# Kernel optimization log

Measured on AMD Instinct MI355X. Metric: run time of the kernel, lower is better.

## Reference

```python
import jax, jax.numpy as jnp
import numpy as np

# MiniCPM3 MLA attention dims
HIDDEN = 2560
N_HEADS = 40
Q_LORA = 768
KV_LORA = 256
ROPE_D = 32
NOPE_D = 64
V_D = HIDDEN // N_HEADS          # 64
Q_HEAD_D = NOPE_D + ROPE_D       # 96
ROPE_BASE = 10000.0
EPS = 1e-6


def setup_inputs() -> dict:
    key = jax.random.key(0)
    ks = jax.random.split(key, 8)
    B, S = 1, 2048
    sc = lambda fan_in: 1.0 / np.sqrt(fan_in)
    return {
        "hidden_states": jax.random.normal(ks[0], (B, S, HIDDEN), jnp.float32),
        "position_ids": jnp.arange(B * S, dtype=jnp.int64).reshape(B, S) % S,
        "w_qa": jax.random.normal(ks[1], (HIDDEN, Q_LORA), jnp.float32) * sc(HIDDEN),
        "q_a_ln_w": jnp.ones((Q_LORA,), jnp.float32),
        "w_qb": jax.random.normal(ks[2], (Q_LORA, N_HEADS * Q_HEAD_D), jnp.float32) * sc(Q_LORA),
        "w_kva": jax.random.normal(ks[3], (HIDDEN, KV_LORA + ROPE_D), jnp.float32) * sc(HIDDEN),
        "kv_a_ln_w": jnp.ones((KV_LORA,), jnp.float32),
        "w_kvb": jax.random.normal(ks[4], (KV_LORA, N_HEADS * (NOPE_D + V_D)), jnp.float32) * sc(KV_LORA),
        "w_o": jax.random.normal(ks[5], (N_HEADS * V_D, HIDDEN), jnp.float32) * sc(N_HEADS * V_D),
    }


def _rmsnorm(x, w, eps=EPS):
    var = jnp.mean(x * x, axis=-1, keepdims=True)
    return x * jax.lax.rsqrt(var + eps) * w


def _rotate_half(x):
    h = x.shape[-1] // 2
    return jnp.concatenate([-x[..., h:], x[..., :h]], axis=-1)


def _rope_cache(seq_len, dim, base, dtype=jnp.float32):
    inv_freq = 1.0 / (base ** (jnp.arange(0, dim, 2, dtype=jnp.float32) / dim))
    t = jnp.arange(seq_len, dtype=jnp.float32)
    freqs = jnp.outer(t, inv_freq)                      # [S, dim/2]
    emb = jnp.concatenate([freqs, freqs], axis=-1)      # [S, dim]
    return jnp.cos(emb).astype(dtype), jnp.sin(emb).astype(dtype)


def reference(hidden_states, position_ids, w_qa, q_a_ln_w, w_qb, w_kva, kv_a_ln_w, w_kvb, w_o):
    B, S, _ = hidden_states.shape
    # --- low-rank Q projection: a -> RMSNorm -> b ---
    q = _rmsnorm(hidden_states @ w_qa, q_a_ln_w) @ w_qb          # [B,S,H*96]
    q = q.reshape(B, S, N_HEADS, Q_HEAD_D).transpose(0, 2, 1, 3)  # [B,H,S,96]
    q_nope, q_pe = q[..., :NOPE_D], q[..., NOPE_D:]
    # --- compressed KV + shared rope key ---
    ckv = hidden_states @ w_kva                                   # [B,S,256+32]
    compressed_kv, k_pe = ckv[..., :KV_LORA], ckv[..., KV_LORA:]
    k_pe = k_pe[:, None, :, :]                                    # [B,1,S,32]
    kv = _rmsnorm(compressed_kv, kv_a_ln_w) @ w_kvb               # [B,S,H*(64+64)]
    kv = kv.reshape(B, S, N_HEADS, NOPE_D + V_D).transpose(0, 2, 1, 3)
    k_nope, v = kv[..., :NOPE_D], kv[..., NOPE_D:]                # [B,H,S,64] each
    # --- RoPE on the 32-dim rope sub-dimension (fp32, as original) ---
    cos, sin = _rope_cache(S, ROPE_D, ROPE_BASE)
    cos = cos[position_ids][:, None, :, :]                        # [B,1,S,32]
    sin = sin[position_ids][:, None, :, :]
    q_pe = q_pe * cos + _rotate_half(q_pe) * sin
    k_pe = k_pe * cos + _rotate_half(k_pe) * sin
    # --- concat nope/rope parts ---
    q_full = jnp.concatenate([q_nope, q_pe], axis=-1)             # [B,H,S,96]
    k_full = jnp.concatenate([k_nope, jnp.broadcast_to(k_pe, (B, N_HEADS, S, ROPE_D))], axis=-1)
    # --- causal SDPA with scale q_head_dim**-0.5 ---
    scale = Q_HEAD_D ** -0.5
    scores = jnp.einsum("bhqd,bhkd->bhqk", q_full, k_full) * scale
    causal = jnp.tril(jnp.ones((S, S), bool))
    scores = jnp.where(causal, scores, jnp.finfo(scores.dtype).min)
    probs = jax.nn.softmax(scores, axis=-1)
    attn = jnp.einsum("bhqk,bhkd->bhqd", probs, v)                # [B,H,S,64]
    attn = attn.transpose(0, 2, 1, 3).reshape(B, S, N_HEADS * V_D)
    return attn @ w_o
```

## Files before the change

kernel.cpp:

```cpp
#include <hip/hip_runtime.h>
#include <hip/hip_bf16.h>

typedef __hip_bfloat16 bf16;
typedef __attribute__((ext_vector_type(8))) __bf16 bf16x8;
typedef __attribute__((ext_vector_type(4))) __bf16 bf16x4;
typedef __attribute__((ext_vector_type(4))) float f32x4;

constexpr int S_LEN = 2048;
constexpr int HID   = 2560;
constexpr int NH    = 40;
constexpr int QL    = 768;
constexpr int KVL   = 256;
constexpr int RD    = 32;
constexpr int ND    = 64;
constexpr int VD    = 64;
constexpr int QHD   = 96;
constexpr int QB_N  = NH * QHD;
constexpr int KVB_N = NH * (ND + VD);
constexpr int CKV_N = KVL + RD;
constexpr int AB_N  = QL + CKV_N;

#define MFMA16(a, b, c) __builtin_amdgcn_mfma_f32_16x16x32_bf16((a), (b), (c), 0, 0, 0)

__device__ __forceinline__ int get_pos(const int* pos, int s) {
  bool is64 = (pos[1] == 0 && pos[2] == 1);
  return is64 ? pos[2 * s] : pos[s];
}


__global__ void cast_f32_bf16(const float* __restrict__ src, bf16* __restrict__ dst, int n4) {
  int i = blockIdx.x * blockDim.x + threadIdx.x;
  if (i >= n4) return;
  float4 v = reinterpret_cast<const float4*>(src)[i];
  struct { bf16 a, b, c, d; } pk;
  pk.a = __float2bfloat16(v.x); pk.b = __float2bfloat16(v.y);
  pk.c = __float2bfloat16(v.z); pk.d = __float2bfloat16(v.w);
  reinterpret_cast<uint2*>(dst)[i] = *reinterpret_cast<uint2*>(&pk);
}

__global__ void transpose_cast(const float* __restrict__ src, bf16* __restrict__ dst, int K, int N) {
  __shared__ float tile[32][33];
  int nb = blockIdx.x * 32, kb = blockIdx.y * 32;
  int x = threadIdx.x, y = threadIdx.y;
#pragma unroll
  for (int j = 0; j < 4; ++j) {
    int k = kb + y + j * 8, n = nb + x;
    tile[y + j * 8][x] = (k < K && n < N) ? src[(size_t)k * N + n] : 0.f;
  }
  __syncthreads();
#pragma unroll
  for (int j = 0; j < 4; ++j) {
    int n = nb + y + j * 8, k = kb + x;
    if (n < N && k < K) dst[(size_t)n * K + k] = __float2bfloat16(tile[x][y + j * 8]);
  }
}


template<bool OBF16, bool NEDGE>
__global__ __launch_bounds__(256) void gemm_bt(const bf16* __restrict__ A,
                                               const bf16* __restrict__ B,
                                               void* __restrict__ Cv,
                                               int M, int N, int K) {
  constexpr int BM = 128, BN = 128, BK = 64;
  __shared__ __bf16 ldsA[BM * BK];
  __shared__ __bf16 ldsB[BN * BK];
  const int t = threadIdx.x;
  const int l = t & 63, w = t >> 6;
  const int lr = l & 15, lk = l >> 4;
  const int wr = w >> 1, wc = w & 1;
  const int rowbase = blockIdx.y * BM;
  const int colbase = blockIdx.x * BN;

  f32x4 acc[4][4];
#pragma unroll
  for (int m = 0; m < 4; ++m)
#pragma unroll
    for (int n = 0; n < 4; ++n) acc[m][n] = f32x4{0.f, 0.f, 0.f, 0.f};

  const int kiters = K / BK;
  for (int kt = 0; kt < kiters; ++kt) {
    const int kb = kt * BK;
#pragma unroll
    for (int it = 0; it < 4; ++it) {
      const int r  = it * 32 + w * 8 + (l >> 3);
      const int c8 = ((l & 7) * 8) ^ ((r & 7) << 3);
      const bf16* ga = A + (size_t)(rowbase + r) * K + kb + c8;
      __builtin_amdgcn_global_load_lds((const __attribute__((address_space(1))) void*)ga,
          (__attribute__((address_space(3))) void*)(ldsA + it * 2048 + w * 512), 16, 0, 0);
      int nrow = colbase + r;
      if (NEDGE) nrow = (nrow < N) ? nrow : (N - 1);
      const bf16* gb = B + (size_t)nrow * K + kb + c8;
      __builtin_amdgcn_global_load_lds((const __attribute__((address_space(1))) void*)gb,
          (__attribute__((address_space(3))) void*)(ldsB + it * 2048 + w * 512), 16, 0, 0);
    }
    __syncthreads();
#pragma unroll
    for (int kk = 0; kk < 2; ++kk) {
      bf16x8 af[4], bfr[4];
#pragma unroll
      for (int m = 0; m < 4; ++m) {
        const int row = wr * 64 + m * 16 + lr;
        const int ce  = (kk * 32 + lk * 8) ^ ((row & 7) << 3);
        af[m] = *(const bf16x8*)(ldsA + row * BK + ce);
      }
#pragma unroll
      for (int n = 0; n < 4; ++n) {
        const int row = wc * 64 + n * 16 + lr;
        const int ce  = (kk * 32 + lk * 8) ^ ((row & 7) << 3);
        bfr[n] = *(const bf16x8*)(ldsB + row * BK + ce);
      }
#pragma unroll
      for (int m = 0; m < 4; ++m)
#pragma unroll
        for (int n = 0; n < 4; ++n)
          acc[m][n] = MFMA16(af[m], bfr[n], acc[m][n]);
    }
    __syncthreads();
  }

#pragma unroll
  for (int m = 0; m < 4; ++m)
#pragma unroll
    for (int n = 0; n < 4; ++n) {
      const int col = colbase + wc * 64 + n * 16 + lr;
      if (NEDGE && col >= N) continue;
#pragma unroll
      for (int i = 0; i < 4; ++i) {
        const int row = rowbase + wr * 64 + m * 16 + lk * 4 + i;
        if (OBF16) ((bf16*)Cv)[(size_t)row * N + col] = __float2bfloat16(acc[m][n][i]);
        else       ((float*)Cv)[(size_t)row * N + col] = acc[m][n][i];
      }
    }
}

__global__ __launch_bounds__(256) void gemm_qakva(const bf16* __restrict__ A,
                                                  const bf16* __restrict__ B,
                                                  float* __restrict__ q_out,
                                                  float* __restrict__ ckv_out) {
  constexpr int BM = 128, BK = 64, K = HID, N = AB_N;
  __shared__ __bf16 ldsA[BM * BK];
  __shared__ __bf16 ldsB[64 * BK];
  const int t = threadIdx.x;
  const int l = t & 63, w = t >> 6;
  const int lr = l & 15, lk = l >> 4;
  const int rowbase = blockIdx.y * BM;
  const int colbase = blockIdx.x * 64;

  f32x4 acc[2][4];
#pragma unroll
  for (int m = 0; m < 2; ++m)
#pragma unroll
    for (int n = 0; n < 4; ++n) acc[m][n] = f32x4{0.f, 0.f, 0.f, 0.f};

  for (int kt = 0; kt < K / BK; ++kt) {
    const int kb = kt * BK;
#pragma unroll
    for (int it = 0; it < 4; ++it) {
      const int r  = it * 32 + w * 8 + (l >> 3);
      const int c8 = ((l & 7) * 8) ^ ((r & 7) << 3);
      const bf16* ga = A + (size_t)(rowbase + r) * K + kb + c8;
      __builtin_amdgcn_global_load_lds((const __attribute__((address_space(1))) void*)ga,
          (__attribute__((address_space(3))) void*)(ldsA + it * 2048 + w * 512), 16, 0, 0);
      if (it < 2) {
        int nrow = colbase + r;
        nrow = (nrow < N) ? nrow : (N - 1);
        const bf16* gb = B + (size_t)nrow * K + kb + c8;
        __builtin_amdgcn_global_load_lds((const __attribute__((address_space(1))) void*)gb,
            (__attribute__((address_space(3))) void*)(ldsB + it * 2048 + w * 512), 16, 0, 0);
      }
    }
    __syncthreads();
#pragma unroll
    for (int kk = 0; kk < 2; ++kk) {
      bf16x8 af[2], bfr[4];
#pragma unroll
      for (int m = 0; m < 2; ++m) {
        const int row = w * 32 + m * 16 + lr;
        const int ce  = (kk * 32 + lk * 8) ^ ((row & 7) << 3);
        af[m] = *(const bf16x8*)(ldsA + row * BK + ce);
      }
#pragma unroll
      for (int n = 0; n < 4; ++n) {
        const int row = n * 16 + lr;
        const int ce  = (kk * 32 + lk * 8) ^ ((row & 7) << 3);
        bfr[n] = *(const bf16x8*)(ldsB + row * BK + ce);
      }
#pragma unroll
      for (int m = 0; m < 2; ++m)
#pragma unroll
        for (int n = 0; n < 4; ++n)
          acc[m][n] = MFMA16(af[m], bfr[n], acc[m][n]);
    }
    __syncthreads();
  }

#pragma unroll
  for (int m = 0; m < 2; ++m)
#pragma unroll
    for (int n = 0; n < 4; ++n) {
      const int col = colbase + n * 16 + lr;
#pragma unroll
      for (int i = 0; i < 4; ++i) {
        const int row = rowbase + w * 32 + m * 16 + lk * 4 + i;
        if (col < QL)       q_out[(size_t)row * QL + col] = acc[m][n][i];
        else if (col < N)   ckv_out[(size_t)row * CKV_N + (col - QL)] = acc[m][n][i];
      }
    }
}

__global__ __launch_bounds__(256) void gemm_qb_rope(const bf16* __restrict__ A,
                                                    const bf16* __restrict__ B,
                                                    const float* __restrict__ ropc,
                                                    const float* __restrict__ rops,
                                                    bf16* __restrict__ qfull) {
  constexpr int BM = 128, BN = 128, BK = 64, K = QL, N = QB_N;
  __shared__ __bf16 ldsA[BM * BK];
  __shared__ __bf16 ldsB[BN * BK];
  const int t = threadIdx.x;
  const int l = t & 63, w = t >> 6;
  const int lr = l & 15, lk = l >> 4;
  const int wr = w >> 1, wc = w & 1;
  const int rowbase = blockIdx.y * BM;
  const int colbase = blockIdx.x * BN;
  const float scale = 0.14724444f;

  f32x4 acc[4][4];
#pragma unroll
  for (int m = 0; m < 4; ++m)
#pragma unroll
    for (int n = 0; n < 4; ++n) acc[m][n] = f32x4{0.f, 0.f, 0.f, 0.f};

  for (int kt = 0; kt < K / BK; ++kt) {
    const int kb = kt * BK;
#pragma unroll
    for (int it = 0; it < 4; ++it) {
      const int r  = it * 32 + w * 8 + (l >> 3);
      const int c8 = ((l & 7) * 8) ^ ((r & 7) << 3);
      const bf16* ga = A + (size_t)(rowbase + r) * K + kb + c8;
      __builtin_amdgcn_global_load_lds((const __attribute__((address_space(1))) void*)ga,
          (__attribute__((address_space(3))) void*)(ldsA + it * 2048 + w * 512), 16, 0, 0);
      const bf16* gb = B + (size_t)(colbase + r) * K + kb + c8;
      __builtin_amdgcn_global_load_lds((const __attribute__((address_space(1))) void*)gb,
          (__attribute__((address_space(3))) void*)(ldsB + it * 2048 + w * 512), 16, 0, 0);
    }
    __syncthreads();
#pragma unroll
    for (int kk = 0; kk < 2; ++kk) {
      bf16x8 af[4], bfr[4];
#pragma unroll
      for (int m = 0; m < 4; ++m) {
        const int row = wr * 64 + m * 16 + lr;
        const int ce  = (kk * 32 + lk * 8) ^ ((row & 7) << 3);
        af[m] = *(const bf16x8*)(ldsA + row * BK + ce);
      }
#pragma unroll
      for (int n = 0; n < 4; ++n) {
        const int row = wc * 64 + n * 16 + lr;
        const int ce  = (kk * 32 + lk * 8) ^ ((row & 7) << 3);
        bfr[n] = *(const bf16x8*)(ldsB + row * BK + ce);
      }
#pragma unroll
      for (int m = 0; m < 4; ++m)
#pragma unroll
        for (int n = 0; n < 4; ++n)
          acc[m][n] = MFMA16(af[m], bfr[n], acc[m][n]);
    }
    __syncthreads();
  }

#pragma unroll
  for (int m = 0; m < 4; ++m) {
    const int rowtop = rowbase + wr * 64 + m * 16 + lk * 4;
#pragma unroll
    for (int n = 0; n < 4; ++n) {
      const int c0 = colbase + wc * 64 + n * 16;
      const int h  = c0 / 96;
      const int d0 = c0 - h * 96;
      const size_t qb_ = ((size_t)h * S_LEN + rowtop) * QHD + d0 + lr;
      if (d0 < ND) {
#pragma unroll
        for (int i = 0; i < 4; ++i)
          qfull[qb_ + (size_t)i * QHD] = __float2bfloat16(acc[m][n][i] * scale);
      } else if (d0 == ND) {
#pragma unroll
        for (int i = 0; i < 4; ++i) {
          const float c = ropc[(rowtop + i) * 16 + lr];
          const float s = rops[(rowtop + i) * 16 + lr];
          const float x0 = acc[m][n][i], x1 = acc[m][n + 1][i];
          qfull[qb_ + (size_t)i * QHD] = __float2bfloat16((x0 * c - x1 * s) * scale);
        }
      } else {
#pragma unroll
        for (int i = 0; i < 4; ++i) {
          const float c = ropc[(rowtop + i) * 16 + lr];
          const float s = rops[(rowtop + i) * 16 + lr];
          const float x1 = acc[m][n][i], x0 = acc[m][n - 1][i];
          qfull[qb_ + (size_t)i * QHD] = __float2bfloat16((x1 * c + x0 * s) * scale);
        }
      }
    }
  }
}

__global__ __launch_bounds__(256) void gemm_kvb_split(const bf16* __restrict__ A,
                                                      const bf16* __restrict__ B,
                                                      bf16* __restrict__ knope,
                                                      bf16* __restrict__ vt) {
  constexpr int BM = 128, BN = 128, BK = 64, K = KVL;
  __shared__ __bf16 ldsA[BM * BK];
  __shared__ __bf16 ldsB[BN * BK];
  const int t = threadIdx.x;
  const int l = t & 63, w = t >> 6;
  const int lr = l & 15, lk = l >> 4;
  const int wr = w >> 1, wc = w & 1;
  const int rowbase = blockIdx.y * BM;
  const int h = blockIdx.x;
  const int colbase = h * BN;

  f32x4 acc[4][4];
#pragma unroll
  for (int m = 0; m < 4; ++m)
#pragma unroll
    for (int n = 0; n < 4; ++n) acc[m][n] = f32x4{0.f, 0.f, 0.f, 0.f};

  for (int kt = 0; kt < K / BK; ++kt) {
    const int kb = kt * BK;
#pragma unroll
    for (int it = 0; it < 4; ++it) {
      const int r  = it * 32 + w * 8 + (l >> 3);
      const int c8 = ((l & 7) * 8) ^ ((r & 7) << 3);
      const bf16* ga = A + (size_t)(rowbase + r) * K + kb + c8;
      __builtin_amdgcn_global_load_lds((const __attribute__((address_space(1))) void*)ga,
          (__attribute__((address_space(3))) void*)(ldsA + it * 2048 + w * 512), 16, 0, 0);
      const bf16* gb = B + (size_t)(colbase + r) * K + kb + c8;
      __builtin_amdgcn_global_load_lds((const __attribute__((address_space(1))) void*)gb,
          (__attribute__((address_space(3))) void*)(ldsB + it * 2048 + w * 512), 16, 0, 0);
    }
    __syncthreads();
#pragma unroll
    for (int kk = 0; kk < 2; ++kk) {
      bf16x8 af[4], bfr[4];
#pragma unroll
      for (int m = 0; m < 4; ++m) {
        const int row = wr * 64 + m * 16 + lr;
        const int ce  = (kk * 32 + lk * 8) ^ ((row & 7) << 3);
        af[m] = *(const bf16x8*)(ldsA + row * BK + ce);
      }
#pragma unroll
      for (int n = 0; n < 4; ++n) {
        const int row = wc * 64 + n * 16 + lr;
        const int ce  = (kk * 32 + lk * 8) ^ ((row & 7) << 3);
        bfr[n] = *(const bf16x8*)(ldsB + row * BK + ce);
      }
#pragma unroll
      for (int m = 0; m < 4; ++m)
#pragma unroll
        for (int n = 0; n < 4; ++n)
          acc[m][n] = MFMA16(af[m], bfr[n], acc[m][n]);
    }
    __syncthreads();
  }

#pragma unroll
  for (int m = 0; m < 4; ++m) {
    const int rowtop = rowbase + wr * 64 + m * 16 + lk * 4;
    if (wc == 0) {
#pragma unroll
      for (int n = 0; n < 4; ++n) {
        const int d = n * 16 + lr;
#pragma unroll
        for (int i = 0; i < 4; ++i)
          knope[((size_t)h * S_LEN + rowtop + i) * ND + d] = __float2bfloat16(acc[m][n][i]);
      }
    } else {
#pragma unroll
      for (int n = 0; n < 4; ++n) {
        const int d = n * 16 + lr;
        bf16x4 pk;
#pragma unroll
        for (int i = 0; i < 4; ++i) pk[i] = (__bf16)acc[m][n][i];
        *(bf16x4*)(vt + ((size_t)h * VD + d) * S_LEN + rowtop) = pk;
      }
    }
  }
}


__global__ void rmsnorm_rows(const float* __restrict__ in, const float* __restrict__ w,
                             bf16* __restrict__ out, int C) {
  const int r = blockIdx.x;
  const float* row = in + (size_t)r * C;
  float ss = 0.f;
  for (int c = threadIdx.x; c < C; c += 256) { float v = row[c]; ss += v * v; }
#pragma unroll
  for (int d = 32; d > 0; d >>= 1) ss += __shfl_xor(ss, d);
  __shared__ float red[4];
  if ((threadIdx.x & 63) == 0) red[threadIdx.x >> 6] = ss;
  __syncthreads();
  const float tot = red[0] + red[1] + red[2] + red[3];
  const float rs = rsqrtf(tot / (float)C + 1e-6f);
  for (int c = threadIdx.x; c < C; c += 256)
    out[(size_t)r * C + c] = __float2bfloat16(row[c] * rs * w[c]);
}

__global__ void kv_prep(const float* __restrict__ ckv, const float* __restrict__ w,
                        const int* __restrict__ pos, bf16* __restrict__ ckv_bf,
                        bf16* __restrict__ kpe, float* __restrict__ ropc,
                        float* __restrict__ rops) {
  const int s = blockIdx.x, t = threadIdx.x;
  const float* row = ckv + (size_t)s * CKV_N;
  float v[4]; float ss = 0.f;
#pragma unroll
  for (int j = 0; j < 4; ++j) { v[j] = row[t + 64 * j]; ss += v[j] * v[j]; }
#pragma unroll
  for (int d = 32; d > 0; d >>= 1) ss += __shfl_xor(ss, d);
  const float rs = rsqrtf(ss / (float)KVL + 1e-6f);
#pragma unroll
  for (int j = 0; j < 4; ++j)
    ckv_bf[(size_t)s * KVL + t + 64 * j] = __float2bfloat16(v[j] * rs * w[t + 64 * j]);
  if (t < 16) {
    const float x0 = row[KVL + t], x1 = row[KVL + 16 + t];
    const float p = (float)get_pos(pos, s);
    const float invf = exp2f(-(float)t * (13.2877124f / 16.f));
    const float ang = p * invf, c = cosf(ang), sn = sinf(ang);
    ropc[s * 16 + t] = c;
    rops[s * 16 + t] = sn;
    kpe[(size_t)s * RD + t]      = __float2bfloat16(x0 * c - x1 * sn);
    kpe[(size_t)s * RD + 16 + t] = __float2bfloat16(x1 * c + x0 * sn);
  }
}

__global__ __launch_bounds__(64) void attn_kernel(const bf16* __restrict__ qfull,
                                                  const bf16* __restrict__ knope,
                                                  const bf16* __restrict__ kpe,
                                                  const bf16* __restrict__ vt,
                                                  bf16* __restrict__ ctx) {
  const int h = blockIdx.x;
  const int qw = ((int)gridDim.y - 1 - (int)blockIdx.y) * 32;
  const int l = threadIdx.x;
  const int lr = l & 15, lk = l >> 4;
  const bf16* Q  = qfull + (size_t)h * S_LEN * QHD;
  const bf16* Kn = knope + (size_t)h * S_LEN * ND;
  const bf16* V  = vt + (size_t)h * VD * S_LEN;
  __shared__ __bf16 plds[32][64];

  bf16x8 qf[2][3];
#pragma unroll
  for (int qg = 0; qg < 2; ++qg)
#pragma unroll
    for (int ks = 0; ks < 3; ++ks)
      qf[qg][ks] = *(const bf16x8*)(Q + (size_t)(qw + qg * 16 + lr) * QHD + ks * 32 + lk * 8);

  f32x4 o[2][4];
  float mrow[2], lrow[2];
#pragma unroll
  for (int qg = 0; qg < 2; ++qg) {
#pragma unroll
    for (int dt = 0; dt < 4; ++dt) o[qg][dt] = f32x4{0.f, 0.f, 0.f, 0.f};
    mrow[qg] = -1e30f; lrow[qg] = 0.f;
  }

  bf16x8 kf[4][3];
#pragma unroll
  for (int sub = 0; sub < 4; ++sub) {
#pragma unroll
    for (int ks = 0; ks < 2; ++ks)
      kf[sub][ks] = *(const bf16x8*)(Kn + (size_t)(sub * 16 + lr) * ND + ks * 32 + lk * 8);
    kf[sub][2] = *(const bf16x8*)(kpe + (size_t)(sub * 16 + lr) * RD + lk * 8);
  }

  for (int kb = 0;; kb += 64) {
    f32x4 st[2][4];
#pragma unroll
    for (int qg = 0; qg < 2; ++qg)
#pragma unroll
      for (int sub = 0; sub < 4; ++sub) st[qg][sub] = f32x4{0.f, 0.f, 0.f, 0.f};
#pragma unroll
    for (int qg = 0; qg < 2; ++qg)
#pragma unroll
      for (int sub = 0; sub < 4; ++sub)
#pragma unroll
        for (int ks = 0; ks < 3; ++ks)
          st[qg][sub] = MFMA16(kf[sub][ks], qf[qg][ks], st[qg][sub]);

    const int nkb = kb + 64;
    if (nkb <= qw) {
#pragma unroll
      for (int sub = 0; sub < 4; ++sub) {
#pragma unroll
        for (int ks = 0; ks < 2; ++ks)
          kf[sub][ks] = *(const bf16x8*)(Kn + (size_t)(nkb + sub * 16 + lr) * ND + ks * 32 + lk * 8);
        kf[sub][2] = *(const bf16x8*)(kpe + (size_t)(nkb + sub * 16 + lr) * RD + lk * 8);
      }
    }

    const bool diag = (kb + 64 > qw);
    float tm[2];
#pragma unroll
    for (int qg = 0; qg < 2; ++qg) {
      const int q = qw + qg * 16 + lr;
      if (diag) {
#pragma unroll
        for (int sub = 0; sub < 4; ++sub)
#pragma unroll
          for (int i = 0; i < 4; ++i)
            if (kb + sub * 16 + lk * 4 + i > q) st[qg][sub][i] = -1e30f;
      }
      float m0 = -1e30f;
#pragma unroll
      for (int sub = 0; sub < 4; ++sub)
#pragma unroll
        for (int i = 0; i < 4; ++i) m0 = fmaxf(m0, st[qg][sub][i]);
      m0 = fmaxf(m0, __shfl_xor(m0, 16));
      m0 = fmaxf(m0, __shfl_xor(m0, 32));
      tm[qg] = m0;
    }

    const bool noresc = __all((tm[0] <= mrow[0] + 8.f) && (tm[1] <= mrow[1] + 8.f));
    float fac[2];
#pragma unroll
    for (int qg = 0; qg < 2; ++qg) {
      const float mnew = noresc ? mrow[qg] : fmaxf(mrow[qg], tm[qg]);
      float ts = 0.f;
#pragma unroll
      for (int sub = 0; sub < 4; ++sub) {
        bf16x4 pk;
#pragma unroll
        for (int i = 0; i < 4; ++i) {
          const float p = exp2f(st[qg][sub][i] - mnew);
          ts += p;
          pk[i] = (__bf16)p;
        }
        const int swc = (sub * 16 + lk * 4) ^ ((lr & 7) << 3);
        *(bf16x4*)(&plds[qg * 16 + lr][swc]) = pk;
      }
      ts += __shfl_xor(ts, 16);
      ts += __shfl_xor(ts, 32);
      if (noresc) {
        lrow[qg] += ts;
      } else {
        fac[qg] = exp2f(mrow[qg] - mnew);
        lrow[qg] = lrow[qg] * fac[qg] + ts;
        mrow[qg] = mnew;
      }
    }
    if (!noresc) {
#pragma unroll
      for (int qg = 0; qg < 2; ++qg)
#pragma unroll
        for (int i = 0; i < 4; ++i) {
          const float fr = __shfl(fac[qg], lk * 4 + i);
#pragma unroll
          for (int dt = 0; dt < 4; ++dt) o[qg][dt][i] *= fr;
        }
    }

#pragma unroll
    for (int h2 = 0; h2 < 2; ++h2) {
      const int swc = (h2 * 32 + lk * 8) ^ ((lr & 7) << 3);
      bf16x8 pa0 = *(const bf16x8*)(&plds[lr][swc]);
      bf16x8 pa1 = *(const bf16x8*)(&plds[16 + lr][swc]);
#pragma unroll
      for (int dt = 0; dt < 4; ++dt) {
        bf16x8 vf = *(const bf16x8*)(V + (size_t)(dt * 16 + lr) * S_LEN + kb + h2 * 32 + lk * 8);
        o[0][dt] = MFMA16(pa0, vf, o[0][dt]);
        o[1][dt] = MFMA16(pa1, vf, o[1][dt]);
      }
    }
    if (nkb > qw) break;
  }

#pragma unroll
  for (int qg = 0; qg < 2; ++qg) {
    const float linv = 1.0f / lrow[qg];
#pragma unroll
    for (int i = 0; i < 4; ++i) {
      const float inv = __shfl(linv, lk * 4 + i);
#pragma unroll
      for (int dt = 0; dt < 4; ++dt) {
        const int row = qw + qg * 16 + lk * 4 + i;
        const int col = h * VD + dt * 16 + lr;
        ctx[(size_t)row * HID + col] = __float2bfloat16(o[qg][dt][i] * inv);
      }
    }
  }
}


extern "C" void kernel_launch(void* const* d_in, const int* in_sizes, int n_in,
                              void* d_out, int out_size, void* d_ws, size_t ws_size,
                              hipStream_t stream) {
  const float* hidden = (const float*)d_in[0];
  const int*   pos    = (const int*)d_in[1];
  const float* w_qa   = (const float*)d_in[2];
  const float* q_ln   = (const float*)d_in[3];
  const float* w_qb   = (const float*)d_in[4];
  const float* w_kva  = (const float*)d_in[5];
  const float* kv_ln  = (const float*)d_in[6];
  const float* w_kvb  = (const float*)d_in[7];
  const float* w_o    = (const float*)d_in[8];
  float* out = (float*)d_out;
  char* ws = (char*)d_ws;
  (void)in_sizes; (void)n_in; (void)out_size; (void)ws_size;

  size_t off = 0;
  auto take = [&](size_t bytes) -> char* {
    char* p = ws + off;
    off = (off + bytes + 255) & ~(size_t)255;
    return p;
  };
  bf16*  hid_bf = (bf16*)take((size_t)S_LEN * HID * 2);
  bf16*  wabT   = (bf16*)take((size_t)AB_N * HID * 2);
  bf16*  wqbT   = (bf16*)take((size_t)QB_N * QL * 2);
  bf16*  wkvbT  = (bf16*)take((size_t)KVB_N * KVL * 2);
  bf16*  woT    = (bf16*)take((size_t)HID * HID * 2);
  float* qlora  = (float*)take((size_t)S_LEN * QL * 4);
  bf16*  qa_bf  = (bf16*)take((size_t)S_LEN * QL * 2);
  bf16*  qfull  = (bf16*)take((size_t)NH * S_LEN * QHD * 2);
  float* ckv    = (float*)take((size_t)S_LEN * CKV_N * 4);
  bf16*  ckv_bf = (bf16*)take((size_t)S_LEN * KVL * 2);
  bf16*  kpe    = (bf16*)take((size_t)S_LEN * RD * 2);
  float* ropc   = (float*)take((size_t)S_LEN * 16 * 4);
  float* rops   = (float*)take((size_t)S_LEN * 16 * 4);
  bf16*  knope  = (bf16*)take((size_t)NH * S_LEN * ND * 2);
  bf16*  vt     = (bf16*)take((size_t)NH * VD * S_LEN * 2);
  bf16*  ctx    = (bf16*)take((size_t)S_LEN * HID * 2);

  const dim3 tb(32, 8);
  cast_f32_bf16<<<(S_LEN * HID / 4 + 255) / 256, 256, 0, stream>>>(hidden, hid_bf, S_LEN * HID / 4);
  transpose_cast<<<dim3((QL + 31) / 32, (HID + 31) / 32), tb, 0, stream>>>(w_qa, wabT, HID, QL);
  transpose_cast<<<dim3((CKV_N + 31) / 32, (HID + 31) / 32), tb, 0, stream>>>(w_kva, wabT + (size_t)QL * HID, HID, CKV_N);
  transpose_cast<<<dim3((QB_N + 31) / 32, (QL + 31) / 32), tb, 0, stream>>>(w_qb, wqbT, QL, QB_N);
  transpose_cast<<<dim3((KVB_N + 31) / 32, (KVL + 31) / 32), tb, 0, stream>>>(w_kvb, wkvbT, KVL, KVB_N);
  transpose_cast<<<dim3((HID + 31) / 32, (HID + 31) / 32), tb, 0, stream>>>(w_o, woT, HID, HID);

  gemm_qakva<<<dim3((AB_N + 63) / 64, S_LEN / 128), 256, 0, stream>>>(hid_bf, wabT, qlora, ckv);

  kv_prep<<<S_LEN, 64, 0, stream>>>(ckv, kv_ln, pos, ckv_bf, kpe, ropc, rops);

  rmsnorm_rows<<<S_LEN, 256, 0, stream>>>(qlora, q_ln, qa_bf, QL);
  gemm_qb_rope<<<dim3(QB_N / 128, S_LEN / 128), 256, 0, stream>>>(qa_bf, wqbT, ropc, rops, qfull);

  gemm_kvb_split<<<dim3(KVB_N / 128, S_LEN / 128), 256, 0, stream>>>(ckv_bf, wkvbT, knope, vt);

  attn_kernel<<<dim3(NH, S_LEN / 32), 64, 0, stream>>>(qfull, knope, kpe, vt, ctx);
  gemm_bt<false, false><<<dim3(HID / 128, S_LEN / 128), 256, 0, stream>>>(ctx, woT, out, S_LEN, HID, HID);
}
```

Baseline: 267.3 us.

## Rebalance causal attention work by pairing short and long query tiles per wave

```diff
diff --git a/kernel.cpp b/kernel.cpp
--- a/kernel.cpp
+++ b/kernel.cpp
@@ -430,157 +430,136 @@
   }
 }
 
-__global__ __launch_bounds__(64) void attn_kernel(const bf16* __restrict__ qfull,
-                                                  const bf16* __restrict__ knope,
-                                                  const bf16* __restrict__ kpe,
-                                                  const bf16* __restrict__ vt,
-                                                  bf16* __restrict__ ctx) {
+__global__ __launch_bounds__(256) void attn_kernel(const bf16* __restrict__ qfull,
+                                                   const bf16* __restrict__ knope,
+                                                   const bf16* __restrict__ kpe,
+                                                   const bf16* __restrict__ vt,
+                                                   bf16* __restrict__ ctx) {
   const int h = blockIdx.x;
-  const int qw = ((int)gridDim.y - 1 - (int)blockIdx.y) * 32;
-  const int l = threadIdx.x;
+  const int w = threadIdx.x >> 6, l = threadIdx.x & 63;
+  const int p = blockIdx.y * 4 + w;
   const int lr = l & 15, lk = l >> 4;
   const bf16* Q  = qfull + (size_t)h * S_LEN * QHD;
   const bf16* Kn = knope + (size_t)h * S_LEN * ND;
   const bf16* V  = vt + (size_t)h * VD * S_LEN;
-  __shared__ __bf16 plds[32][64];
-
-  bf16x8 qf[2][3];
-#pragma unroll
-  for (int qg = 0; qg < 2; ++qg)
+  __shared__ __bf16 plds[4][16][64];
+
+#pragma unroll
+  for (int half = 0; half < 2; ++half) {
+    const int j  = half ? p : (127 - p);
+    const int qw = j * 16;
+    const int lastkb = (qw / 64) * 64;
+
+    bf16x8 qf[3];
 #pragma unroll
     for (int ks = 0; ks < 3; ++ks)
-      qf[qg][ks] = *(const bf16x8*)(Q + (size_t)(qw + qg * 16 + lr) * QHD + ks * 32 + lk * 8);
-
-  f32x4 o[2][4];
-  float mrow[2], lrow[2];
-#pragma unroll
-  for (int qg = 0; qg < 2; ++qg) {
-#pragma unroll
-    for (int dt = 0; dt < 4; ++dt) o[qg][dt] = f32x4{0.f, 0.f, 0.f, 0.f};
-    mrow[qg] = -1e30f; lrow[qg] = 0.f;
-  }
-
-  bf16x8 kf[4][3];
-#pragma unroll
-  for (int sub = 0; sub < 4; ++sub) {
-#pragma unroll
-    for (int ks = 0; ks < 2; ++ks)
-      kf[sub][ks] = *(const bf16x8*)(Kn + (size_t)(sub * 16 + lr) * ND + ks * 32 + lk * 8);
-    kf[sub][2] = *(const bf16x8*)(kpe + (size_t)(sub * 16 + lr) * RD + lk * 8);
-  }
-
-  for (int kb = 0;; kb += 64) {
-    f32x4 st[2][4];
-#pragma unroll
-    for (int qg = 0; qg < 2; ++qg)
-#pragma unroll
-      for (int sub = 0; sub < 4; ++sub) st[qg][sub] = f32x4{0.f, 0.f, 0.f, 0.f};
-#pragma unroll
-    for (int qg = 0; qg < 2; ++qg)
+      qf[ks] = *(const bf16x8*)(Q + (size_t)(qw + lr) * QHD + ks * 32 + lk * 8);
+
+    f32x4 o[4];
+#pragma unroll
+    for (int dt = 0; dt < 4; ++dt) o[dt] = f32x4{0.f, 0.f, 0.f, 0.f};
+    float mrow = -1e30f, lrow = 0.f;
+
+    bf16x8 kf[4][3];
+#pragma unroll
+    for (int sub = 0; sub < 4; ++sub) {
+#pragma unroll
+      for (int ks = 0; ks < 2; ++ks)
+        kf[sub][ks] = *(const bf16x8*)(Kn + (size_t)(sub * 16 + lr) * ND + ks * 32 + lk * 8);
+      kf[sub][2] = *(const bf16x8*)(kpe + (size_t)(sub * 16 + lr) * RD + lk * 8);
+    }
+
+    for (int kb = 0;; kb += 64) {
+      f32x4 st[4];
+#pragma unroll
+      for (int sub = 0; sub < 4; ++sub) st[sub] = f32x4{0.f, 0.f, 0.f, 0.f};
 #pragma unroll
       for (int sub = 0; sub < 4; ++sub)
 #pragma unroll
         for (int ks = 0; ks < 3; ++ks)
-          st[qg][sub] = MFMA16(kf[sub][ks], qf[qg][ks], st[qg][sub]);
-
-    const int nkb = kb + 64;
-    if (nkb <= qw) {
-#pragma unroll
-      for (int sub = 0; sub < 4; ++sub) {
-#pragma unroll
-        for (int ks = 0; ks < 2; ++ks)
-          kf[sub][ks] = *(const bf16x8*)(Kn + (size_t)(nkb + sub * 16 + lr) * ND + ks * 32 + lk * 8);
-        kf[sub][2] = *(const bf16x8*)(kpe + (size_t)(nkb + sub * 16 + lr) * RD + lk * 8);
-      }
-    }
-
-    const bool diag = (kb + 64 > qw);
-    float tm[2];
-#pragma unroll
-    for (int qg = 0; qg < 2; ++qg) {
-      const int q = qw + qg * 16 + lr;
-      if (diag) {
+          st[sub] = MFMA16(kf[sub][ks], qf[ks], st[sub]);
+
+      const int nkb = kb + 64;
+      if (nkb <= lastkb) {
+#pragma unroll
+        for (int sub = 0; sub < 4; ++sub) {
+#pragma unroll
+          for (int ks = 0; ks < 2; ++ks)
+            kf[sub][ks] = *(const bf16x8*)(Kn + (size_t)(nkb + sub * 16 + lr) * ND + ks * 32 + lk * 8);
+          kf[sub][2] = *(const bf16x8*)(kpe + (size_t)(nkb + sub * 16 + lr) * RD + lk * 8);
+        }
+      }
+
+      if (kb == lastkb) {
+        const int q = qw + lr;
 #pragma unroll
         for (int sub = 0; sub < 4; ++sub)
 #pragma unroll
           for (int i = 0; i < 4; ++i)
-            if (kb + sub * 16 + lk * 4 + i > q) st[qg][sub][i] = -1e30f;
-      }
+            if (kb + sub * 16 + lk * 4 + i > q) st[sub][i] = -1e30f;
+      }
+
       float m0 = -1e30f;
 #pragma unroll
       for (int sub = 0; sub < 4; ++sub)
 #pragma unroll
-        for (int i = 0; i < 4; ++i) m0 = fmaxf(m0, st[qg][sub][i]);
+        for (int i = 0; i < 4; ++i) m0 = fmaxf(m0, st[sub][i]);
       m0 = fmaxf(m0, __shfl_xor(m0, 16));
       m0 = fmaxf(m0, __shfl_xor(m0, 32));
-      tm[qg] = m0;
-    }
-
-    const bool noresc = __all((tm[0] <= mrow[0] + 8.f) && (tm[1] <= mrow[1] + 8.f));
-    float fac[2];
-#pragma unroll
-    for (int qg = 0; qg < 2; ++qg) {
-      const float mnew = noresc ? mrow[qg] : fmaxf(mrow[qg], tm[qg]);
+
+      const bool noresc = __all(m0 <= mrow + 8.f);
+      const float mnew = noresc ? mrow : fmaxf(mrow, m0);
       float ts = 0.f;
 #pragma unroll
       for (int sub = 0; sub < 4; ++sub) {
         bf16x4 pk;
 #pragma unroll
         for (int i = 0; i < 4; ++i) {
-          const float p = exp2f(st[qg][sub][i] - mnew);
-          ts += p;
-          pk[i] = (__bf16)p;
+          const float pv = exp2f(st[sub][i] - mnew);
+          ts += pv;
+          pk[i] = (__bf16)pv;
         }
         const int swc = (sub * 16 + lk * 4) ^ ((lr & 7) << 3);
-        *(bf16x4*)(&plds[qg * 16 + lr][swc]) = pk;
+        *(bf16x4*)(&plds[w][lr][swc]) = pk;
       }
       ts += __shfl_xor(ts, 16);
       ts += __shfl_xor(ts, 32);
       if (noresc) {
-        lrow[qg] += ts;
+        lrow += ts;
       } else {
-        fac[qg] = exp2f(mrow[qg] - mnew);
-        lrow[qg] = lrow[qg] * fac[qg] + ts;
-        mrow[qg] = mnew;
-      }
-    }
-    if (!noresc) {
-#pragma unroll
-      for (int qg = 0; qg < 2; ++qg)
+        const float fac = exp2f(mrow - mnew);
+        lrow = lrow * fac + ts;
+        mrow = mnew;
 #pragma unroll
         for (int i = 0; i < 4; ++i) {
-          const float fr = __shfl(fac[qg], lk * 4 + i);
-#pragma unroll
-          for (int dt = 0; dt < 4; ++dt) o[qg][dt][i] *= fr;
+          const float fr = __shfl(fac, lk * 4 + i);
+#pragma unroll
+          for (int dt = 0; dt < 4; ++dt) o[dt][i] *= fr;
         }
-    }
-
-#pragma unroll
-    for (int h2 = 0; h2 < 2; ++h2) {
-      const int swc = (h2 * 32 + lk * 8) ^ ((lr & 7) << 3);
-      bf16x8 pa0 = *(const bf16x8*)(&plds[lr][swc]);
-      bf16x8 pa1 = *(const bf16x8*)(&plds[16 + lr][swc]);
-#pragma unroll
-      for (int dt = 0; dt < 4; ++dt) {
-        bf16x8 vf = *(const bf16x8*)(V + (size_t)(dt * 16 + lr) * S_LEN + kb + h2 * 32 + lk * 8);
-        o[0][dt] = MFMA16(pa0, vf, o[0][dt]);
-        o[1][dt] = MFMA16(pa1, vf, o[1][dt]);
-      }
-    }
-    if (nkb > qw) break;
-  }
-
-#pragma unroll
-  for (int qg = 0; qg < 2; ++qg) {
-    const float linv = 1.0f / lrow[qg];
+      }
+
+#pragma unroll
+      for (int h2 = 0; h2 < 2; ++h2) {
+        const int swc = (h2 * 32 + lk * 8) ^ ((lr & 7) << 3);
+        bf16x8 pa = *(const bf16x8*)(&plds[w][lr][swc]);
+#pragma unroll
+        for (int dt = 0; dt < 4; ++dt) {
+          bf16x8 vf = *(const bf16x8*)(V + (size_t)(dt * 16 + lr) * S_LEN + kb + h2 * 32 + lk * 8);
+          o[dt] = MFMA16(pa, vf, o[dt]);
+        }
+      }
+      if (kb == lastkb) break;
+    }
+
+    const float linv = 1.0f / lrow;
 #pragma unroll
     for (int i = 0; i < 4; ++i) {
       const float inv = __shfl(linv, lk * 4 + i);
 #pragma unroll
       for (int dt = 0; dt < 4; ++dt) {
-        const int row = qw + qg * 16 + lk * 4 + i;
+        const int row = qw + lk * 4 + i;
         const int col = h * VD + dt * 16 + lr;
-        ctx[(size_t)row * HID + col] = __float2bfloat16(o[qg][dt][i] * inv);
+        ctx[(size_t)row * HID + col] = __float2bfloat16(o[dt][i] * inv);
       }
     }
   }
@@ -643,6 +622,6 @@
 
   gemm_kvb_split<<<dim3(KVB_N / 128, S_LEN / 128), 256, 0, stream>>>(ckv_bf, wkvbT, knope, vt);
 
-  attn_kernel<<<dim3(NH, S_LEN / 32), 64, 0, stream>>>(qfull, knope, kpe, vt, ctx);
+  attn_kernel<<<dim3(NH, 16), 256, 0, stream>>>(qfull, knope, kpe, vt, ctx);
   gemm_bt<false, false><<<dim3(HID / 128, S_LEN / 128), 256, 0, stream>>>(ctx, woT, out, S_LEN, HID, HID);
 }
```

Result: slower. 364.9 us (+36.5%).

## Share K tiles across four attention waves via async LDS double buffering

Applied to the files above, without the earlier changes.

```diff
diff --git a/kernel.cpp b/kernel.cpp
--- a/kernel.cpp
+++ b/kernel.cpp
@@ -368,9 +368,13 @@
 #pragma unroll
       for (int n = 0; n < 4; ++n) {
         const int d = n * 16 + lr;
-#pragma unroll
-        for (int i = 0; i < 4; ++i)
-          knope[((size_t)h * S_LEN + rowtop + i) * ND + d] = __float2bfloat16(acc[m][n][i]);
+        const int chunk = d >> 3, dlo = d & 7;
+#pragma unroll
+        for (int i = 0; i < 4; ++i) {
+          const int s = rowtop + i;
+          const int dsw = ((chunk ^ (s & 7)) << 3) + dlo;
+          knope[((size_t)h * S_LEN + s) * ND + dsw] = __float2bfloat16(acc[m][n][i]);
+        }
       }
     } else {
 #pragma unroll
@@ -430,19 +434,23 @@
   }
 }
 
-__global__ __launch_bounds__(64) void attn_kernel(const bf16* __restrict__ qfull,
-                                                  const bf16* __restrict__ knope,
-                                                  const bf16* __restrict__ kpe,
-                                                  const bf16* __restrict__ vt,
-                                                  bf16* __restrict__ ctx) {
+__global__ __launch_bounds__(256) void attn_kernel(const bf16* __restrict__ qfull,
+                                                   const bf16* __restrict__ knope,
+                                                   const bf16* __restrict__ kpe,
+                                                   const bf16* __restrict__ vt,
+                                                   bf16* __restrict__ ctx) {
   const int h = blockIdx.x;
-  const int qw = ((int)gridDim.y - 1 - (int)blockIdx.y) * 32;
-  const int l = threadIdx.x;
+  const int qb = ((int)gridDim.y - 1 - (int)blockIdx.y) * 128;
+  const int t = threadIdx.x, w = t >> 6, l = t & 63;
   const int lr = l & 15, lk = l >> 4;
+  const int qw = qb + w * 32;
+  const int lastw = (qw >> 6) << 6;
+  const int last3 = ((qb + 96) >> 6) << 6;
   const bf16* Q  = qfull + (size_t)h * S_LEN * QHD;
   const bf16* Kn = knope + (size_t)h * S_LEN * ND;
   const bf16* V  = vt + (size_t)h * VD * S_LEN;
-  __shared__ __bf16 plds[32][64];
+  __shared__ __bf16 kbuf[2][64 * ND];
+  __shared__ __bf16 plds[4][32][64];
 
   bf16x8 qf[2][3];
 #pragma unroll
@@ -460,114 +468,142 @@
     mrow[qg] = -1e30f; lrow[qg] = 0.f;
   }
 
-  bf16x8 kf[4][3];
-#pragma unroll
-  for (int sub = 0; sub < 4; ++sub) {
-#pragma unroll
-    for (int ks = 0; ks < 2; ++ks)
-      kf[sub][ks] = *(const bf16x8*)(Kn + (size_t)(sub * 16 + lr) * ND + ks * 32 + lk * 8);
-    kf[sub][2] = *(const bf16x8*)(kpe + (size_t)(sub * 16 + lr) * RD + lk * 8);
-  }
+  auto stage = [&](int buf, int kb) {
+    const bf16* src = Kn + (size_t)kb * ND + w * 512 + l * 8;
+    __bf16* dst = &kbuf[buf][w * 512];
+#pragma unroll
+    for (int i = 0; i < 2; ++i)
+      __builtin_amdgcn_global_load_lds((const __attribute__((address_space(1))) void*)(src + i * 2048),
+          (__attribute__((address_space(3))) void*)(dst + i * 2048), 16, 0, 0);
+  };
+
+  stage(0, 0);
+  bf16x8 pe[4];
+#pragma unroll
+  for (int sub = 0; sub < 4; ++sub)
+    pe[sub] = *(const bf16x8*)(kpe + (size_t)(sub * 16 + lr) * RD + lk * 8);
+  __syncthreads();
 
   for (int kb = 0;; kb += 64) {
-    f32x4 st[2][4];
-#pragma unroll
-    for (int qg = 0; qg < 2; ++qg)
-#pragma unroll
-      for (int sub = 0; sub < 4; ++sub) st[qg][sub] = f32x4{0.f, 0.f, 0.f, 0.f};
-#pragma unroll
-    for (int qg = 0; qg < 2; ++qg)
-#pragma unroll
-      for (int sub = 0; sub < 4; ++sub)
-#pragma unroll
-        for (int ks = 0; ks < 3; ++ks)
-          st[qg][sub] = MFMA16(kf[sub][ks], qf[qg][ks], st[qg][sub]);
-
-    const int nkb = kb + 64;
-    if (nkb <= qw) {
+    const int cur = (kb >> 6) & 1;
+    if (kb + 64 <= last3) stage(cur ^ 1, kb + 64);
+
+    if (kb <= lastw) {
+      bf16x8 kfn[4][2];
 #pragma unroll
       for (int sub = 0; sub < 4; ++sub) {
-#pragma unroll
-        for (int ks = 0; ks < 2; ++ks)
-          kf[sub][ks] = *(const bf16x8*)(Kn + (size_t)(nkb + sub * 16 + lr) * ND + ks * 32 + lk * 8);
-        kf[sub][2] = *(const bf16x8*)(kpe + (size_t)(nkb + sub * 16 + lr) * RD + lk * 8);
-      }
-    }
-
-    const bool diag = (kb + 64 > qw);
-    float tm[2];
-#pragma unroll
-    for (int qg = 0; qg < 2; ++qg) {
-      const int q = qw + qg * 16 + lr;
-      if (diag) {
+        const int row = sub * 16 + lr;
+#pragma unroll
+        for (int ks = 0; ks < 2; ++ks) {
+          const int ch = ((ks * 4 + lk) ^ (lr & 7)) << 3;
+          kfn[sub][ks] = *(const bf16x8*)(&kbuf[cur][row * ND + ch]);
+        }
+      }
+
+      f32x4 st[2][4];
+#pragma unroll
+      for (int qg = 0; qg < 2; ++qg)
+#pragma unroll
+        for (int sub = 0; sub < 4; ++sub) st[qg][sub] = f32x4{0.f, 0.f, 0.f, 0.f};
+#pragma unroll
+      for (int qg = 0; qg < 2; ++qg)
+#pragma unroll
+        for (int sub = 0; sub < 4; ++sub) {
+          st[qg][sub] = MFMA16(kfn[sub][0], qf[qg][0], st[qg][sub]);
+          st[qg][sub] = MFMA16(kfn[sub][1], qf[qg][1], st[qg][sub]);
+          st[qg][sub] = MFMA16(pe[sub],     qf[qg][2], st[qg][sub]);
+        }
+
+      const int nkb = kb + 64;
+      bf16x8 pen[4];
+      if (nkb <= lastw) {
 #pragma unroll
         for (int sub = 0; sub < 4; ++sub)
-#pragma unroll
-          for (int i = 0; i < 4; ++i)
-            if (kb + sub * 16 + lk * 4 + i > q) st[qg][sub][i] = -1e30f;
-      }
-      float m0 = -1e30f;
-#pragma unroll
-      for (int sub = 0; sub < 4; ++sub)
-#pragma unroll
-        for (int i = 0; i < 4; ++i) m0 = fmaxf(m0, st[qg][sub][i]);
-      m0 = fmaxf(m0, __shfl_xor(m0, 16));
-      m0 = fmaxf(m0, __shfl_xor(m0, 32));
-      tm[qg] = m0;
-    }
-
-    const bool noresc = __all((tm[0] <= mrow[0] + 8.f) && (tm[1] <= mrow[1] + 8.f));
-    float fac[2];
-#pragma unroll
-    for (int qg = 0; qg < 2; ++qg) {
-      const float mnew = noresc ? mrow[qg] : fmaxf(mrow[qg], tm[qg]);
-      float ts = 0.f;
-#pragma unroll
-      for (int sub = 0; sub < 4; ++sub) {
-        bf16x4 pk;
-#pragma unroll
-        for (int i = 0; i < 4; ++i) {
-          const float p = exp2f(st[qg][sub][i] - mnew);
-          ts += p;
-          pk[i] = (__bf16)p;
-        }
-        const int swc = (sub * 16 + lk * 4) ^ ((lr & 7) << 3);
-        *(bf16x4*)(&plds[qg * 16 + lr][swc]) = pk;
-      }
-      ts += __shfl_xor(ts, 16);
-      ts += __shfl_xor(ts, 32);
-      if (noresc) {
-        lrow[qg] += ts;
-      } else {
-        fac[qg] = exp2f(mrow[qg] - mnew);
-        lrow[qg] = lrow[qg] * fac[qg] + ts;
-        mrow[qg] = mnew;
-      }
-    }
-    if (!noresc) {
-#pragma unroll
-      for (int qg = 0; qg < 2; ++qg)
-#pragma unroll
-        for (int i = 0; i < 4; ++i) {
-          const float fr = __shfl(fac[qg], lk * 4 + i);
-#pragma unroll
-          for (int dt = 0; dt < 4; ++dt) o[qg][dt][i] *= fr;
-        }
-    }
-
-#pragma unroll
-    for (int h2 = 0; h2 < 2; ++h2) {
-      const int swc = (h2 * 32 + lk * 8) ^ ((lr & 7) << 3);
-      bf16x8 pa0 = *(const bf16x8*)(&plds[lr][swc]);
-      bf16x8 pa1 = *(const bf16x8*)(&plds[16 + lr][swc]);
-#pragma unroll
-      for (int dt = 0; dt < 4; ++dt) {
-        bf16x8 vf = *(const bf16x8*)(V + (size_t)(dt * 16 + lr) * S_LEN + kb + h2 * 32 + lk * 8);
-        o[0][dt] = MFMA16(pa0, vf, o[0][dt]);
-        o[1][dt] = MFMA16(pa1, vf, o[1][dt]);
-      }
-    }
-    if (nkb > qw) break;
+          pen[sub] = *(const bf16x8*)(kpe + (size_t)(nkb + sub * 16 + lr) * RD + lk * 8);
+      }
+
+      const bool diag = (kb == lastw);
+      float tm[2];
+#pragma unroll
+      for (int qg = 0; qg < 2; ++qg) {
+        const int q = qw + qg * 16 + lr;
+        if (diag) {
+#pragma unroll
+          for (int sub = 0; sub < 4; ++sub)
+#pragma unroll
+            for (int i = 0; i < 4; ++i)
+              if (kb + sub * 16 + lk * 4 + i > q) st[qg][sub][i] = -1e30f;
+        }
+        float m0 = -1e30f;
+#pragma unroll
+        for (int sub = 0; sub < 4; ++sub)
+#pragma unroll
+          for (int i = 0; i < 4; ++i) m0 = fmaxf(m0, st[qg][sub][i]);
+        m0 = fmaxf(m0, __shfl_xor(m0, 16));
+        m0 = fmaxf(m0, __shfl_xor(m0, 32));
+        tm[qg] = m0;
+      }
+
+      const bool noresc = __all((tm[0] <= mrow[0] + 8.f) && (tm[1] <= mrow[1] + 8.f));
+      float fac[2];
+#pragma unroll
+      for (int qg = 0; qg < 2; ++qg) {
+        const float mnew = noresc ? mrow[qg] : fmaxf(mrow[qg], tm[qg]);
+        float ts = 0.f;
+#pragma unroll
+        for (int sub = 0; sub < 4; ++sub) {
+          bf16x4 pk;
+#pragma unroll
+          for (int i = 0; i < 4; ++i) {
+            const float pv = exp2f(st[qg][sub][i] - mnew);
+            ts += pv;
+            pk[i] = (__bf16)pv;
+          }
+          const int swc = (sub * 16 + lk * 4) ^ ((lr & 7) << 3);
+          *(bf16x4*)(&plds[w][qg * 16 + lr][swc]) = pk;
+        }
+        ts += __shfl_xor(ts, 16);
+        ts += __shfl_xor(ts, 32);
+        if (noresc) {
+          lrow[qg] += ts;
+        } else {
+          fac[qg] = exp2f(mrow[qg] - mnew);
+          lrow[qg] = lrow[qg] * fac[qg] + ts;
+          mrow[qg] = mnew;
+        }
+      }
+      if (!noresc) {
+#pragma unroll
+        for (int qg = 0; qg < 2; ++qg)
+#pragma unroll
+          for (int i = 0; i < 4; ++i) {
+            const float fr = __shfl(fac[qg], lk * 4 + i);
+#pragma unroll
+            for (int dt = 0; dt < 4; ++dt) o[qg][dt][i] *= fr;
+          }
+      }
+
+#pragma unroll
+      for (int h2 = 0; h2 < 2; ++h2) {
+        const int swc = (h2 * 32 + lk * 8) ^ ((lr & 7) << 3);
+        bf16x8 pa0 = *(const bf16x8*)(&plds[w][lr][swc]);
+        bf16x8 pa1 = *(const bf16x8*)(&plds[w][16 + lr][swc]);
+#pragma unroll
+        for (int dt = 0; dt < 4; ++dt) {
+          bf16x8 vf = *(const bf16x8*)(V + (size_t)(dt * 16 + lr) * S_LEN + kb + h2 * 32 + lk * 8);
+          o[0][dt] = MFMA16(pa0, vf, o[0][dt]);
+          o[1][dt] = MFMA16(pa1, vf, o[1][dt]);
+        }
+      }
+
+      if (nkb <= lastw) {
+#pragma unroll
+        for (int sub = 0; sub < 4; ++sub) pe[sub] = pen[sub];
+      }
+    }
+
+    __syncthreads();
+    if (kb == last3) break;
   }
 
 #pragma unroll
@@ -643,6 +679,6 @@
 
   gemm_kvb_split<<<dim3(KVB_N / 128, S_LEN / 128), 256, 0, stream>>>(ckv_bf, wkvbT, knope, vt);
 
-  attn_kernel<<<dim3(NH, S_LEN / 32), 64, 0, stream>>>(qfull, knope, kpe, vt, ctx);
+  attn_kernel<<<dim3(NH, 16), 256, 0, stream>>>(qfull, knope, kpe, vt, ctx);
   gemm_bt<false, false><<<dim3(HID / 128, S_LEN / 128), 256, 0, stream>>>(ctx, woT, out, S_LEN, HID, HID);
 }
```

Result: no change. 268.0 us (+0.3%).

## Split long causal attention rows across two blocks and merge with combine kernel

Applied to the files above, without the earlier changes.

```diff
diff --git a/kernel.cpp b/kernel.cpp
--- a/kernel.cpp
+++ b/kernel.cpp
@@ -434,11 +434,24 @@
                                                   const bf16* __restrict__ knope,
                                                   const bf16* __restrict__ kpe,
                                                   const bf16* __restrict__ vt,
-                                                  bf16* __restrict__ ctx) {
-  const int h = blockIdx.x;
-  const int qw = ((int)gridDim.y - 1 - (int)blockIdx.y) * 32;
-  const int l = threadIdx.x;
-  const int lr = l & 15, lk = l >> 4;
+                                                  bf16* __restrict__ ctx,
+                                                  float* __restrict__ osc,
+                                                  float* __restrict__ msc,
+                                                  float* __restrict__ lsc) {
+  const int i = blockIdx.x;
+  int h, j; bool isB;
+  if (i < 1280) { h = i % 40; j = 63 - i / 40; isB = true; }
+  else { const int i2 = i - 1280; h = i2 % 40; j = 63 - i2 / 40; isB = false; }
+  const int ktiles = j / 2 + 1;
+  const bool split = (j >= 32);
+  const int nA = (ktiles + 1) >> 1;
+  const int kt0 = (split && isB) ? nA : 0;
+  const int kt1 = (split && !isB) ? nA : ktiles;
+  const int kb0 = kt0 * 64;
+  const int kbLast = (kt1 - 1) * 64;
+  const int lastkb = (ktiles - 1) * 64;
+  const int qw = j * 32;
+  const int l = threadIdx.x, lr = l & 15, lk = l >> 4;
   const bf16* Q  = qfull + (size_t)h * S_LEN * QHD;
   const bf16* Kn = knope + (size_t)h * S_LEN * ND;
   const bf16* V  = vt + (size_t)h * VD * S_LEN;
@@ -451,13 +464,18 @@
     for (int ks = 0; ks < 3; ++ks)
       qf[qg][ks] = *(const bf16x8*)(Q + (size_t)(qw + qg * 16 + lr) * QHD + ks * 32 + lk * 8);
 
-  f32x4 o[2][4];
-  float mrow[2], lrow[2];
+  bf16x8 ones;
+#pragma unroll
+  for (int c = 0; c < 8; ++c) ones[c] = (__bf16)1.0f;
+
+  f32x4 o[2][4], lac[2];
+  float mrow[2];
 #pragma unroll
   for (int qg = 0; qg < 2; ++qg) {
 #pragma unroll
     for (int dt = 0; dt < 4; ++dt) o[qg][dt] = f32x4{0.f, 0.f, 0.f, 0.f};
-    mrow[qg] = -1e30f; lrow[qg] = 0.f;
+    lac[qg] = f32x4{0.f, 0.f, 0.f, 0.f};
+    mrow[qg] = -1e30f;
   }
 
   bf16x8 kf[4][3];
@@ -465,11 +483,11 @@
   for (int sub = 0; sub < 4; ++sub) {
 #pragma unroll
     for (int ks = 0; ks < 2; ++ks)
-      kf[sub][ks] = *(const bf16x8*)(Kn + (size_t)(sub * 16 + lr) * ND + ks * 32 + lk * 8);
-    kf[sub][2] = *(const bf16x8*)(kpe + (size_t)(sub * 16 + lr) * RD + lk * 8);
-  }
-
-  for (int kb = 0;; kb += 64) {
+      kf[sub][ks] = *(const bf16x8*)(Kn + (size_t)(kb0 + sub * 16 + lr) * ND + ks * 32 + lk * 8);
+    kf[sub][2] = *(const bf16x8*)(kpe + (size_t)(kb0 + sub * 16 + lr) * RD + lk * 8);
+  }
+
+  for (int kb = kb0;; kb += 64) {
     f32x4 st[2][4];
 #pragma unroll
     for (int qg = 0; qg < 2; ++qg)
@@ -484,7 +502,7 @@
           st[qg][sub] = MFMA16(kf[sub][ks], qf[qg][ks], st[qg][sub]);
 
     const int nkb = kb + 64;
-    if (nkb <= qw) {
+    if (nkb <= kbLast) {
 #pragma unroll
       for (int sub = 0; sub < 4; ++sub) {
 #pragma unroll
@@ -494,65 +512,59 @@
       }
     }
 
-    const bool diag = (kb + 64 > qw);
+    if (kb == lastkb) {
+#pragma unroll
+      for (int qg = 0; qg < 2; ++qg) {
+        const int q = qw + qg * 16 + lr;
+#pragma unroll
+        for (int sub = 0; sub < 4; ++sub)
+#pragma unroll
+          for (int ii = 0; ii < 4; ++ii)
+            if (kb + sub * 16 + lk * 4 + ii > q) st[qg][sub][ii] = -1e30f;
+      }
+    }
+
     float tm[2];
 #pragma unroll
     for (int qg = 0; qg < 2; ++qg) {
-      const int q = qw + qg * 16 + lr;
-      if (diag) {
-#pragma unroll
-        for (int sub = 0; sub < 4; ++sub)
-#pragma unroll
-          for (int i = 0; i < 4; ++i)
-            if (kb + sub * 16 + lk * 4 + i > q) st[qg][sub][i] = -1e30f;
-      }
       float m0 = -1e30f;
 #pragma unroll
       for (int sub = 0; sub < 4; ++sub)
 #pragma unroll
-        for (int i = 0; i < 4; ++i) m0 = fmaxf(m0, st[qg][sub][i]);
+        for (int ii = 0; ii < 4; ++ii) m0 = fmaxf(m0, st[qg][sub][ii]);
       m0 = fmaxf(m0, __shfl_xor(m0, 16));
       m0 = fmaxf(m0, __shfl_xor(m0, 32));
       tm[qg] = m0;
     }
 
     const bool noresc = __all((tm[0] <= mrow[0] + 8.f) && (tm[1] <= mrow[1] + 8.f));
-    float fac[2];
+    float mnew[2];
 #pragma unroll
     for (int qg = 0; qg < 2; ++qg) {
-      const float mnew = noresc ? mrow[qg] : fmaxf(mrow[qg], tm[qg]);
-      float ts = 0.f;
+      mnew[qg] = noresc ? mrow[qg] : fmaxf(mrow[qg], tm[qg]);
 #pragma unroll
       for (int sub = 0; sub < 4; ++sub) {
         bf16x4 pk;
 #pragma unroll
-        for (int i = 0; i < 4; ++i) {
-          const float p = exp2f(st[qg][sub][i] - mnew);
-          ts += p;
-          pk[i] = (__bf16)p;
-        }
+        for (int ii = 0; ii < 4; ++ii)
+          pk[ii] = (__bf16)exp2f(st[qg][sub][ii] - mnew[qg]);
         const int swc = (sub * 16 + lk * 4) ^ ((lr & 7) << 3);
         *(bf16x4*)(&plds[qg * 16 + lr][swc]) = pk;
       }
-      ts += __shfl_xor(ts, 16);
-      ts += __shfl_xor(ts, 32);
-      if (noresc) {
-        lrow[qg] += ts;
-      } else {
-        fac[qg] = exp2f(mrow[qg] - mnew);
-        lrow[qg] = lrow[qg] * fac[qg] + ts;
-        mrow[qg] = mnew;
-      }
     }
     if (!noresc) {
 #pragma unroll
-      for (int qg = 0; qg < 2; ++qg)
-#pragma unroll
-        for (int i = 0; i < 4; ++i) {
-          const float fr = __shfl(fac[qg], lk * 4 + i);
-#pragma unroll
-          for (int dt = 0; dt < 4; ++dt) o[qg][dt][i] *= fr;
+      for (int qg = 0; qg < 2; ++qg) {
+        const float fac = exp2f(mrow[qg] - mnew[qg]);
+        mrow[qg] = mnew[qg];
+#pragma unroll
+        for (int ii = 0; ii < 4; ++ii) {
+          const float fr = __shfl(fac, lk * 4 + ii);
+#pragma unroll
+          for (int dt = 0; dt < 4; ++dt) o[qg][dt][ii] *= fr;
+          lac[qg][ii] *= fr;
         }
+      }
     }
 
 #pragma unroll
@@ -566,24 +578,66 @@
         o[0][dt] = MFMA16(pa0, vf, o[0][dt]);
         o[1][dt] = MFMA16(pa1, vf, o[1][dt]);
       }
-    }
-    if (nkb > qw) break;
-  }
-
-#pragma unroll
-  for (int qg = 0; qg < 2; ++qg) {
-    const float linv = 1.0f / lrow[qg];
-#pragma unroll
-    for (int i = 0; i < 4; ++i) {
-      const float inv = __shfl(linv, lk * 4 + i);
-#pragma unroll
-      for (int dt = 0; dt < 4; ++dt) {
-        const int row = qw + qg * 16 + lk * 4 + i;
-        const int col = h * VD + dt * 16 + lr;
-        ctx[(size_t)row * HID + col] = __float2bfloat16(o[qg][dt][i] * inv);
-      }
-    }
-  }
+      lac[0] = MFMA16(pa0, ones, lac[0]);
+      lac[1] = MFMA16(pa1, ones, lac[1]);
+    }
+    if (kb == kbLast) break;
+  }
+
+  if (!split) {
+#pragma unroll
+    for (int qg = 0; qg < 2; ++qg)
+#pragma unroll
+      for (int ii = 0; ii < 4; ++ii) {
+        const float inv = 1.0f / lac[qg][ii];
+        const int row = qw + qg * 16 + lk * 4 + ii;
+#pragma unroll
+        for (int dt = 0; dt < 4; ++dt)
+          ctx[(size_t)row * HID + h * VD + dt * 16 + lr] =
+              __float2bfloat16(o[qg][dt][ii] * inv);
+      }
+  } else {
+    const int sidx = h * 32 + (j - 32);
+    const int part = isB ? 1 : 0;
+    const int rbase = (sidx * 2 + part) * 32;
+    float* ob = osc + (size_t)rbase * 64;
+#pragma unroll
+    for (int qg = 0; qg < 2; ++qg)
+#pragma unroll
+      for (int ii = 0; ii < 4; ++ii) {
+        const int row = qg * 16 + lk * 4 + ii;
+#pragma unroll
+        for (int dt = 0; dt < 4; ++dt)
+          ob[(size_t)row * 64 + dt * 16 + lr] = o[qg][dt][ii];
+        if (lr == 0) lsc[rbase + row] = lac[qg][ii];
+      }
+    if (lk == 0) {
+      msc[rbase + lr]      = mrow[0];
+      msc[rbase + 16 + lr] = mrow[1];
+    }
+  }
+}
+
+__global__ __launch_bounds__(256) void attn_combine(const float* __restrict__ osc,
+                                                    const float* __restrict__ msc,
+                                                    const float* __restrict__ lsc,
+                                                    bf16* __restrict__ ctx) {
+  const int sidx = blockIdx.x;
+  const int h = sidx / 32, j = (sidx & 31) + 32;
+  const int t = threadIdx.x;
+  const int row = t >> 3, g = t & 7;
+  const int ra = sidx * 64 + row, rb = ra + 32;
+  const float mA = msc[ra], mB = msc[rb];
+  const float lA = lsc[ra], lB = lsc[rb];
+  const float M = fmaxf(mA, mB);
+  const float wA = exp2f(mA - M), wB = exp2f(mB - M);
+  const float inv = 1.0f / (wA * lA + wB * lB);
+  const float* oA = osc + (size_t)ra * 64 + g * 8;
+  const float* oB = osc + (size_t)rb * 64 + g * 8;
+  bf16* dst = ctx + (size_t)(j * 32 + row) * HID + h * VD + g * 8;
+#pragma unroll
+  for (int c = 0; c < 8; ++c)
+    dst[c] = __float2bfloat16((wA * oA[c] + wB * oB[c]) * inv);
 }
 
 
@@ -625,6 +679,9 @@
   bf16*  knope  = (bf16*)take((size_t)NH * S_LEN * ND * 2);
   bf16*  vt     = (bf16*)take((size_t)NH * VD * S_LEN * 2);
   bf16*  ctx    = (bf16*)take((size_t)S_LEN * HID * 2);
+  float* osc    = (float*)take((size_t)1280 * 2 * 32 * 64 * 4);
+  float* msc    = (float*)take((size_t)1280 * 2 * 32 * 4);
+  float* lsc    = (float*)take((size_t)1280 * 2 * 32 * 4);
 
   const dim3 tb(32, 8);
   cast_f32_bf16<<<(S_LEN * HID / 4 + 255) / 256, 256, 0, stream>>>(hidden, hid_bf, S_LEN * HID / 4);
@@ -643,6 +700,8 @@
 
   gemm_kvb_split<<<dim3(KVB_N / 128, S_LEN / 128), 256, 0, stream>>>(ckv_bf, wkvbT, knope, vt);
 
-  attn_kernel<<<dim3(NH, S_LEN / 32), 64, 0, stream>>>(qfull, knope, kpe, vt, ctx);
+  attn_kernel<<<3840, 64, 0, stream>>>(qfull, knope, kpe, vt, ctx, osc, msc, lsc);
+  attn_combine<<<1280, 256, 0, stream>>>(osc, msc, lsc, ctx);
+
   gemm_bt<false, false><<<dim3(HID / 128, S_LEN / 128), 256, 0, stream>>>(ctx, woT, out, S_LEN, HID, HID);
 }
```

Measured after the change: 264.9 us. No clear change (-0.9%).
